# Performance work log

Hardware: AMD Instinct MI355X
Metric: run time of the kernel (lower is better)

The kernel has to match this reference:

```python
import jax, jax.numpy as jnp
import numpy as np

DIM = 1024
N_HEADS = 16
HEAD_DIM = DIM // N_HEADS
HIDDEN = 4096
EPS = 1e-12


def setup_inputs() -> dict:
    key = jax.random.key(0)
    ks = jax.random.split(key, 12)
    B, S = 2, 2048
    s = 0.02
    inp = {
        "x": jax.random.normal(ks[0], (B, S, DIM), jnp.float32),
        "attn_mask": jnp.ones((B, S), jnp.int32),
        "Wq": jax.random.normal(ks[1], (DIM, DIM), jnp.float32) * s,
        "bq": jnp.zeros((DIM,), jnp.float32),
        "Wk": jax.random.normal(ks[2], (DIM, DIM), jnp.float32) * s,
        "bk": jnp.zeros((DIM,), jnp.float32),
        "Wv": jax.random.normal(ks[3], (DIM, DIM), jnp.float32) * s,
        "bv": jnp.zeros((DIM,), jnp.float32),
        "Wo": jax.random.normal(ks[4], (DIM, DIM), jnp.float32) * s,
        "bo": jnp.zeros((DIM,), jnp.float32),
        "ln1_g": jnp.ones((DIM,), jnp.float32),
        "ln1_b": jnp.zeros((DIM,), jnp.float32),
        "W1": jax.random.normal(ks[5], (DIM, HIDDEN), jnp.float32) * s,
        "b1": jnp.zeros((HIDDEN,), jnp.float32),
        "W2": jax.random.normal(ks[6], (HIDDEN, DIM), jnp.float32) * s,
        "b2": jnp.zeros((DIM,), jnp.float32),
        "ln2_g": jnp.ones((DIM,), jnp.float32),
        "ln2_b": jnp.zeros((DIM,), jnp.float32),
    }
    return inp


def _layernorm(x, g, b):
    mu = jnp.mean(x, axis=-1, keepdims=True)
    var = jnp.mean(jnp.square(x - mu), axis=-1, keepdims=True)
    return (x - mu) * jax.lax.rsqrt(var + EPS) * g + b


def reference(x, attn_mask, Wq, bq, Wk, bk, Wv, bv, Wo, bo,
              ln1_g, ln1_b, W1, b1, W2, b2, ln2_g, ln2_b):
    B, S, D = x.shape
    def split_heads(t):  # (B,S,D) -> (B,H,S,hd)
        return t.reshape(B, S, N_HEADS, HEAD_DIM).transpose(0, 2, 1, 3)
    q = split_heads(x @ Wq + bq) * (1.0 / np.sqrt(HEAD_DIM))
    k = split_heads(x @ Wk + bk)
    v = split_heads(x @ Wv + bv)
    scores = jnp.einsum("bhqd,bhkd->bhqk", q, k)  # (B,H,S,S)
    neg = jnp.finfo(scores.dtype).min
    mask = (attn_mask == 0)[:, None, None, :]  # (B,1,1,S)
    scores = jnp.where(mask, neg, scores)
    weights = jax.nn.softmax(scores, axis=-1)
    ctx = jnp.einsum("bhqk,bhkd->bhqd", weights, v)
    ctx = ctx.transpose(0, 2, 1, 3).reshape(B, S, D)
    sa_out = ctx @ Wo + bo
    sa_out = _layernorm(sa_out + x, ln1_g, ln1_b)
    h = jax.nn.gelu(sa_out @ W1 + b1, approximate=False)
    ffn_out = h @ W2 + b2
    out = _layernorm(ffn_out + sa_out, ln2_g, ln2_b)
    return out
```

## Files before the change

### kernel.cpp

```cpp
#include <hip/hip_runtime.h>


typedef __bf16 bf16x8 __attribute__((ext_vector_type(8)));
typedef float f32x4 __attribute__((ext_vector_type(4)));

#define DIM_ 1024
#define S_LEN 2048
#define NH 16

__device__ __forceinline__ unsigned short f2bf(float f) {
  unsigned u = __float_as_uint(f);
  u = (u + 0x7FFFu + ((u >> 16) & 1u)) >> 16;
  return (unsigned short)u;
}
__device__ __forceinline__ float bf2f(unsigned short h) {
  return __uint_as_float(((unsigned)h) << 16);
}
__device__ __forceinline__ f32x4 mfma16(bf16x8 a, bf16x8 b, f32x4 c) {
  return __builtin_amdgcn_mfma_f32_16x16x32_bf16(a, b, c, 0, 0, 0);
}
__device__ __forceinline__ void gload_lds16(const void* g, void* l) {
  __builtin_amdgcn_global_load_lds(
      (const __attribute__((address_space(1))) void*)g,
      (__attribute__((address_space(3))) void*)l, 16, 0, 0);
}
__device__ __forceinline__ int swz(int row) { return ((row ^ (row >> 3)) & 7) << 3; }

__global__ __launch_bounds__(256) void trans_cvt(
    const float* __restrict__ W, unsigned short* __restrict__ Wt, int K, int N)
{
  __shared__ float tile[64][65];
  const int n0 = blockIdx.x * 64, k0 = blockIdx.y * 64;
  const int tid = threadIdx.x;
  const int tr = tid >> 4, tc = (tid & 15) << 2;
#pragma unroll
  for (int rr = 0; rr < 64; rr += 16) {
    const float4 v = *(const float4*)&W[(size_t)(k0 + tr + rr) * N + n0 + tc];
    tile[tr + rr][tc + 0] = v.x; tile[tr + rr][tc + 1] = v.y;
    tile[tr + rr][tc + 2] = v.z; tile[tr + rr][tc + 3] = v.w;
  }
  __syncthreads();
#pragma unroll
  for (int nn = 0; nn < 64; nn += 16) {
    const int n = tr + nn;
    ushort4 o;
    o.x = f2bf(tile[tc + 0][n]);
    o.y = f2bf(tile[tc + 1][n]);
    o.z = f2bf(tile[tc + 2][n]);
    o.w = f2bf(tile[tc + 3][n]);
    *(ushort4*)&Wt[(size_t)(n0 + n) * K + k0 + tc] = o;
  }
}

__global__ void cvt_bf16(const float* __restrict__ in,
                         unsigned short* __restrict__ out, int n4)
{
  const int i = blockIdx.x * blockDim.x + threadIdx.x;
  if (i >= n4) return;
  const float4 v = ((const float4*)in)[i];
  ushort4 o = { f2bf(v.x), f2bf(v.y), f2bf(v.z), f2bf(v.w) };
  ((ushort4*)out)[i] = o;
}

__global__ __launch_bounds__(256) void trans_v(
    const unsigned short* __restrict__ v, unsigned short* __restrict__ vt)
{
  __shared__ unsigned short tile[64][66];
  const int st = blockIdx.x, bh = blockIdx.y;
  const int tid = threadIdx.x;
  const int r = tid >> 3, c = (tid & 7) << 3;
  const size_t base = (size_t)bh * (S_LEN * 64);
#pragma unroll
  for (int p = 0; p < 2; ++p) {
    const int s = r + p * 32;
    const uint4 raw = *(const uint4*)(v + base + (size_t)(st * 64 + s) * 64 + c);
    const unsigned short* pr = (const unsigned short*)&raw;
#pragma unroll
    for (int j = 0; j < 8; ++j) tile[s][c + j] = pr[j];
  }
  __syncthreads();
#pragma unroll
  for (int p = 0; p < 2; ++p) {
    const int hd = r + p * 32;
    ushort4 o[2];
#pragma unroll
    for (int j = 0; j < 8; ++j) ((unsigned short*)o)[j] = tile[c + j][hd];
    *(uint4*)(vt + (size_t)bh * (64 * S_LEN) + (size_t)hd * S_LEN + st * 64 + c) =
        *(const uint4*)o;
  }
}

template <int EPI>
__global__ __launch_bounds__(256) void gemm_bt(
    const unsigned short* __restrict__ A,
    const unsigned short* __restrict__ Bt,
    const float* __restrict__ bias,
    const float* __restrict__ bias2,
    const float* __restrict__ bias3,
    int N, int K,
    unsigned short* __restrict__ bout)
{
  __shared__ __align__(16) unsigned short As[128 * 64];
  __shared__ __align__(16) unsigned short Bs[128 * 64];
  const int tn = blockIdx.x, tm = blockIdx.y;
  const int tid = threadIdx.x;
  const int wid = tid >> 6, lane = tid & 63;
  const int wm = wid >> 1, wn = wid & 1;
  const int l15 = lane & 15, lg = lane >> 4;
  const int srow = lane >> 3, sk8 = (lane & 7) << 3;

  f32x4 acc[4][4];
#pragma unroll
  for (int i = 0; i < 4; ++i)
#pragma unroll
    for (int j = 0; j < 4; ++j) acc[i][j] = (f32x4){0.f, 0.f, 0.f, 0.f};

  const size_t abase = (size_t)(tm * 128) * K;
  const size_t bbase = (size_t)(tn * 128) * K;

  for (int kk = 0; kk < K; kk += 64) {
    __syncthreads();
#pragma unroll
    for (int s = 0; s < 4; ++s) {
      const int row = wid * 32 + s * 8 + srow;
      const int sw = sk8 ^ swz(row);
      gload_lds16(A + abase + (size_t)row * K + kk + sw, &As[(wid * 32 + s * 8) * 64]);
      gload_lds16(Bt + bbase + (size_t)row * K + kk + sw, &Bs[(wid * 32 + s * 8) * 64]);
    }
    __syncthreads();
#pragma unroll
    for (int sub = 0; sub < 2; ++sub) {
      bf16x8 af[4], bfr[4];
#pragma unroll
      for (int mr = 0; mr < 4; ++mr) {
        const int row = wm * 64 + mr * 16 + l15;
        af[mr] = *(const bf16x8*)&As[row * 64 + ((sub * 32 + lg * 8) ^ swz(row))];
      }
#pragma unroll
      for (int nr = 0; nr < 4; ++nr) {
        const int row = wn * 64 + nr * 16 + l15;
        bfr[nr] = *(const bf16x8*)&Bs[row * 64 + ((sub * 32 + lg * 8) ^ swz(row))];
      }
#pragma unroll
      for (int mr = 0; mr < 4; ++mr)
#pragma unroll
        for (int nr = 0; nr < 4; ++nr)
          acc[mr][nr] = mfma16(af[mr], bfr[nr], acc[mr][nr]);
    }
  }

#pragma unroll
  for (int nr = 0; nr < 4; ++nr) {
    const int col = tn * 128 + wn * 64 + nr * 16 + l15;
    float bv;
    int which = 0, c = col;
    if (EPI == 0) {
      which = col >> 10;
      c = col & 1023;
      const float* bp = (which == 0) ? bias : (which == 1) ? bias2 : bias3;
      bv = bp[c];
    } else {
      bv = bias[col];
    }
#pragma unroll
    for (int mr = 0; mr < 4; ++mr) {
#pragma unroll
      for (int j = 0; j < 4; ++j) {
        const int row = tm * 128 + wm * 64 + mr * 16 + lg * 4 + j;
        float v = acc[mr][nr][j] + bv;
        if (EPI == 0) {
          if (which == 0) v *= 0.125f;
          const int b = row >> 11, s = row & 2047, h = c >> 6, hd = c & 63;
          bout[(size_t)which * 4194304 +
               (((size_t)(b * NH + h)) * S_LEN + s) * 64 + hd] = f2bf(v);
        } else {
          const float gl = 0.5f * v * (1.f + erff(v * 0.70710678118654752f));
          bout[(size_t)row * N + col] = f2bf(gl);
        }
      }
    }
  }
}

template <int EPI>
__global__ __launch_bounds__(256) void gemm64(
    const unsigned short* __restrict__ A,
    const unsigned short* __restrict__ Bt,
    const float* __restrict__ bias,
    int N, int K,
    float* __restrict__ fout,
    const float* __restrict__ resf,
    const unsigned short* __restrict__ resb)
{
  __shared__ __align__(16) unsigned short As[2][64 * 64];
  __shared__ __align__(16) unsigned short Bs[2][128 * 64];
  const int tn = blockIdx.x, tm = blockIdx.y;
  const int tid = threadIdx.x;
  const int wid = tid >> 6, lane = tid & 63;
  const int wm = wid >> 1, wn = wid & 1;
  const int l15 = lane & 15, lg = lane >> 4;
  const int srow = lane >> 3, sk8 = (lane & 7) << 3;

  f32x4 acc[2][4];
#pragma unroll
  for (int i = 0; i < 2; ++i)
#pragma unroll
    for (int j = 0; j < 4; ++j) acc[i][j] = (f32x4){0.f, 0.f, 0.f, 0.f};

  const size_t abase = (size_t)(tm * 64) * K;
  const size_t bbase = (size_t)(tn * 128) * K;

  auto STAGE = [&](int bufn, int kk) {
#pragma unroll
    for (int s = 0; s < 2; ++s) {
      const int row = wid * 16 + s * 8 + srow;
      gload_lds16(A + abase + (size_t)row * K + kk + (sk8 ^ swz(row)),
                  &As[bufn][(wid * 16 + s * 8) * 64]);
    }
#pragma unroll
    for (int s = 0; s < 4; ++s) {
      const int row = wid * 32 + s * 8 + srow;
      gload_lds16(Bt + bbase + (size_t)row * K + kk + (sk8 ^ swz(row)),
                  &Bs[bufn][(wid * 32 + s * 8) * 64]);
    }
  };

  STAGE(0, 0);
  __syncthreads();
  int cur = 0;
  for (int kk = 0; kk < K; kk += 64) {
    if (kk + 64 < K) STAGE(cur ^ 1, kk + 64);
#pragma unroll
    for (int sub = 0; sub < 2; ++sub) {
      bf16x8 af[2], bfr[4];
#pragma unroll
      for (int mr = 0; mr < 2; ++mr) {
        const int row = wm * 32 + mr * 16 + l15;
        af[mr] = *(const bf16x8*)&As[cur][row * 64 + ((sub * 32 + lg * 8) ^ swz(row))];
      }
#pragma unroll
      for (int nr = 0; nr < 4; ++nr) {
        const int row = wn * 64 + nr * 16 + l15;
        bfr[nr] = *(const bf16x8*)&Bs[cur][row * 64 + ((sub * 32 + lg * 8) ^ swz(row))];
      }
#pragma unroll
      for (int mr = 0; mr < 2; ++mr)
#pragma unroll
        for (int nr = 0; nr < 4; ++nr)
          acc[mr][nr] = mfma16(af[mr], bfr[nr], acc[mr][nr]);
    }
    __syncthreads();
    cur ^= 1;
  }

#pragma unroll
  for (int nr = 0; nr < 4; ++nr) {
    const int col = tn * 128 + wn * 64 + nr * 16 + l15;
    const float bv = bias[col];
#pragma unroll
    for (int mr = 0; mr < 2; ++mr) {
#pragma unroll
      for (int j = 0; j < 4; ++j) {
        const int row = tm * 64 + wm * 32 + mr * 16 + lg * 4 + j;
        const float v = acc[mr][nr][j] + bv;
        if (EPI == 1) {
          fout[(size_t)row * N + col] = v + resf[(size_t)row * N + col];
        } else {
          fout[(size_t)row * N + col] = v + bf2f(resb[(size_t)row * N + col]);
        }
      }
    }
  }
}

__global__ __launch_bounds__(512) void attn_fwd(
    const unsigned short* __restrict__ qg,
    const unsigned short* __restrict__ kg,
    const unsigned short* __restrict__ vtg,
    const int* __restrict__ amask,
    unsigned short* __restrict__ ctx)
{
  __shared__ __align__(16) unsigned short Ks[2][64 * 64];
  __shared__ __align__(16) unsigned short Vs[2][64 * 64];
  __shared__ __align__(16) unsigned short Ps[8][16 * 72];
  __shared__ int mk[2][64];

  const int bx = blockIdx.x;
  const int qt = (bx >> 3) & 15;
  const int bh = ((bx & 7) << 2) | (bx >> 7);
  const int b = bh >> 4, h = bh & 15;
  const int tid = threadIdx.x;
  const int wid = tid >> 6, lane = tid & 63;
  const int l15 = lane & 15, lg = lane >> 4;
  const int srow = lane >> 3, sk8 = (lane & 7) << 3;

  const size_t qoff =
      (((size_t)bh * S_LEN) + qt * 128 + wid * 16 + l15) * 64 + lg * 8;
  const bf16x8 aq0 = *(const bf16x8*)&qg[qoff];
  const bf16x8 aq1 = *(const bf16x8*)&qg[qoff + 32];

  f32x4 o_[4];
#pragma unroll
  for (int n = 0; n < 4; ++n) o_[n] = (f32x4){0.f, 0.f, 0.f, 0.f};
  float mj[4]  = {-3e38f, -3e38f, -3e38f, -3e38f};
  float lsj[4] = {0.f, 0.f, 0.f, 0.f};

  const size_t kbase  = (size_t)bh * (S_LEN * 64);
  const size_t vtbase = (size_t)bh * (64 * S_LEN);
  unsigned short* Pw = &Ps[wid][0];
  const int rk = wid * 8 + srow;
  const int swr = sk8 ^ swz(rk);

  auto STAGE = [&](int bufn, int t) {
    gload_lds16(kg + kbase + (size_t)(t * 64 + rk) * 64 + swr,
                &Ks[bufn][wid * 8 * 64]);
    gload_lds16(vtg + vtbase + (size_t)rk * S_LEN + t * 64 + swr,
                &Vs[bufn][wid * 8 * 64]);
    if (tid < 64) mk[bufn][tid] = amask[b * S_LEN + t * 64 + tid];
  };

  STAGE(0, 0);
  __syncthreads();
  int cur = 0;

  for (int t = 0; t < S_LEN / 64; ++t) {
    if (t + 1 < S_LEN / 64) STAGE(cur ^ 1, t + 1);

    f32x4 sf[4];
#pragma unroll
    for (int nr = 0; nr < 4; ++nr) {
      const int kvloc = nr * 16 + l15;
      const int e = swz(kvloc);
      f32x4 a = (f32x4){0.f, 0.f, 0.f, 0.f};
      const bf16x8 bk0 = *(const bf16x8*)&Ks[cur][kvloc * 64 + ((lg * 8) ^ e)];
      const bf16x8 bk1 = *(const bf16x8*)&Ks[cur][kvloc * 64 + ((32 + lg * 8) ^ e)];
      a = mfma16(aq0, bk0, a);
      a = mfma16(aq1, bk1, a);
      sf[nr] = a;
    }
#pragma unroll
    for (int nr = 0; nr < 4; ++nr)
      if (mk[cur][nr * 16 + l15] == 0)
        sf[nr] = (f32x4){-3e38f, -3e38f, -3e38f, -3e38f};

    float pv[4][4];
#pragma unroll
    for (int j = 0; j < 4; ++j) {
      float tmax = fmaxf(fmaxf(sf[0][j], sf[1][j]), fmaxf(sf[2][j], sf[3][j]));
#pragma unroll
      for (int off = 1; off < 16; off <<= 1)
        tmax = fmaxf(tmax, __shfl_xor(tmax, off));
      const float mn = fmaxf(mj[j], tmax);
      const float sc = __expf(mj[j] - mn);
      mj[j] = mn;
      lsj[j] *= sc;
      o_[0][j] *= sc; o_[1][j] *= sc; o_[2][j] *= sc; o_[3][j] *= sc;
#pragma unroll
      for (int nr = 0; nr < 4; ++nr) {
        const float p = __expf(sf[nr][j] - mn);
        pv[nr][j] = p;
        lsj[j] += p;
      }
    }

    asm volatile("s_waitcnt lgkmcnt(0)" ::: "memory");
#pragma unroll
    for (int j = 0; j < 4; ++j) {
      const int qr = lg * 4 + j;
#pragma unroll
      for (int nr = 0; nr < 4; ++nr)
        Pw[qr * 72 + nr * 16 + l15] = f2bf(pv[nr][j]);
    }
    asm volatile("s_waitcnt lgkmcnt(0)" ::: "memory");
    {
      const bf16x8 pa0 = *(const bf16x8*)&Pw[l15 * 72 + lg * 8];
      const bf16x8 pa1 = *(const bf16x8*)&Pw[l15 * 72 + 32 + lg * 8];
#pragma unroll
      for (int n = 0; n < 4; ++n) {
        const int hd = n * 16 + l15;
        const int eh = swz(hd);
        const bf16x8 bv0 = *(const bf16x8*)&Vs[cur][hd * 64 + ((lg * 8) ^ eh)];
        const bf16x8 bv1 = *(const bf16x8*)&Vs[cur][hd * 64 + ((32 + lg * 8) ^ eh)];
        o_[n] = mfma16(pa0, bv0, o_[n]);
        o_[n] = mfma16(pa1, bv1, o_[n]);
      }
    }
    __syncthreads();
    cur ^= 1;
  }

  float rinv[4];
#pragma unroll
  for (int j = 0; j < 4; ++j) {
    float s = lsj[j];
#pragma unroll
    for (int off = 1; off < 16; off <<= 1) s += __shfl_xor(s, off);
    rinv[j] = 1.f / s;
  }
#pragma unroll
  for (int n = 0; n < 4; ++n) {
#pragma unroll
    for (int j = 0; j < 4; ++j) {
      const int sr = qt * 128 + wid * 16 + lg * 4 + j;
      const size_t idx = ((size_t)b * S_LEN + sr) * DIM_ + h * 64 + n * 16 + l15;
      ctx[idx] = f2bf(o_[n][j] * rinv[j]);
    }
  }
}

template <int OUTBF>
__global__ __launch_bounds__(256) void ln_fused(
    const float* __restrict__ in, const float* __restrict__ g,
    const float* __restrict__ be,
    float* __restrict__ fout, unsigned short* __restrict__ bout)
{
  const int row = blockIdx.x, tid = threadIdx.x;
  const float4 v = ((const float4*)(in + (size_t)row * DIM_))[tid];
  float s = v.x + v.y + v.z + v.w;
  float s2 = v.x * v.x + v.y * v.y + v.z * v.z + v.w * v.w;
#pragma unroll
  for (int off = 1; off < 64; off <<= 1) {
    s += __shfl_xor(s, off);
    s2 += __shfl_xor(s2, off);
  }
  __shared__ float rs[4], rs2[4];
  if ((tid & 63) == 0) { rs[tid >> 6] = s; rs2[tid >> 6] = s2; }
  __syncthreads();
  s  = rs[0] + rs[1] + rs[2] + rs[3];
  s2 = rs2[0] + rs2[1] + rs2[2] + rs2[3];
  const float mean = s * (1.f / DIM_);
  const float var = fmaxf(s2 * (1.f / DIM_) - mean * mean, 0.f);
  const float inv = rsqrtf(var + 1e-12f);
  const float4 gv = ((const float4*)g)[tid];
  const float4 bv = ((const float4*)be)[tid];
  const float o0 = (v.x - mean) * inv * gv.x + bv.x;
  const float o1 = (v.y - mean) * inv * gv.y + bv.y;
  const float o2 = (v.z - mean) * inv * gv.z + bv.z;
  const float o3 = (v.w - mean) * inv * gv.w + bv.w;
  if (OUTBF) {
    ushort4 o = { f2bf(o0), f2bf(o1), f2bf(o2), f2bf(o3) };
    ((ushort4*)(bout + (size_t)row * DIM_))[tid] = o;
  } else {
    ((float4*)(fout + (size_t)row * DIM_))[tid] = make_float4(o0, o1, o2, o3);
  }
}

extern "C" void kernel_launch(void* const* d_in, const int* in_sizes, int n_in,
                              void* d_out, int out_size, void* d_ws, size_t ws_size,
                              hipStream_t stream)
{
  const float* x   = (const float*)d_in[0];
  const int* amask = (const int*)d_in[1];
  const float* Wq  = (const float*)d_in[2];
  const float* bq  = (const float*)d_in[3];
  const float* Wk  = (const float*)d_in[4];
  const float* bk  = (const float*)d_in[5];
  const float* Wv  = (const float*)d_in[6];
  const float* bv  = (const float*)d_in[7];
  const float* Wo  = (const float*)d_in[8];
  const float* bo  = (const float*)d_in[9];
  const float* g1  = (const float*)d_in[10];
  const float* be1 = (const float*)d_in[11];
  const float* W1  = (const float*)d_in[12];
  const float* b1  = (const float*)d_in[13];
  const float* W2  = (const float*)d_in[14];
  const float* b2  = (const float*)d_in[15];
  const float* g2  = (const float*)d_in[16];
  const float* be2 = (const float*)d_in[17];
  float* out = (float*)d_out;

  char* ws = (char*)d_ws;
  const size_t MB = (size_t)1 << 20;
  unsigned short* wqkvT = (unsigned short*)(ws + 0 * MB);
  unsigned short* wqt = wqkvT;
  unsigned short* wkt = (unsigned short*)(ws + 2 * MB);
  unsigned short* wvt = (unsigned short*)(ws + 4 * MB);
  unsigned short* wot = (unsigned short*)(ws + 6 * MB);
  unsigned short* w1t = (unsigned short*)(ws + 8 * MB);
  unsigned short* w2t = (unsigned short*)(ws + 16 * MB);
  unsigned short* qb  = (unsigned short*)(ws + 24 * MB);
  unsigned short* xb  = (unsigned short*)(ws + 48 * MB);
  unsigned short* vtb = (unsigned short*)(ws + 48 * MB);
  unsigned short* ctx = (unsigned short*)(ws + 56 * MB);
  unsigned short* sab = qb;
  unsigned short* hb  = (unsigned short*)(ws + 32 * MB);
  float* preln = out;

  trans_cvt<<<dim3(16, 16), 256, 0, stream>>>(Wq, wqt, 1024, 1024);
  trans_cvt<<<dim3(16, 16), 256, 0, stream>>>(Wk, wkt, 1024, 1024);
  trans_cvt<<<dim3(16, 16), 256, 0, stream>>>(Wv, wvt, 1024, 1024);
  trans_cvt<<<dim3(16, 16), 256, 0, stream>>>(Wo, wot, 1024, 1024);
  trans_cvt<<<dim3(64, 16), 256, 0, stream>>>(W1, w1t, 1024, 4096);
  trans_cvt<<<dim3(16, 64), 256, 0, stream>>>(W2, w2t, 4096, 1024);
  cvt_bf16<<<4096, 256, 0, stream>>>(x, xb, 4096 * 1024 / 4);

  gemm_bt<0><<<dim3(24, 32), 256, 0, stream>>>(xb, wqkvT, bq, bk, bv,
      3072, 1024, qb);

  trans_v<<<dim3(32, 32), 256, 0, stream>>>(qb + 2 * 4194304, vtb);

  attn_fwd<<<512, 512, 0, stream>>>(qb, qb + 4194304, vtb, amask, ctx);

  gemm64<1><<<dim3(8, 64), 256, 0, stream>>>(ctx, wot, bo, 1024, 1024,
      preln, x, nullptr);
  ln_fused<1><<<4096, 256, 0, stream>>>(preln, g1, be1, nullptr, sab);

  gemm_bt<2><<<dim3(32, 32), 256, 0, stream>>>(sab, w1t, b1, nullptr, nullptr,
      4096, 1024, hb);
  gemm64<3><<<dim3(8, 64), 256, 0, stream>>>(hb, w2t, b2, 1024, 4096,
      preln, nullptr, sab);
  ln_fused<0><<<4096, 256, 0, stream>>>(preln, g2, be2, out, nullptr);
}
```

Baseline: 406.4 us.

## Transpose QK^T MFMA so softmax row stats are per-lane, add lazy rescale

Swaps the operands of the QK^T MFMA so each lane holds one query row's scores. The running max and sum then need only two cross-lane shuffles instead of a 16-lane butterfly per row. The rescale of the output accumulator is skipped unless the max grows by more than a threshold. P is also stored as packed bf16x4 vectors, and s_setprio is raised around the MFMA sections. Risks are the extra shuffles needed to map per-lane scale factors back onto the O accumulator layout, and bounded precision drift from the lazy rescale threshold.

After: 395.4 us. -2.7%, faster.

```diff
diff --git a/kernel.cpp b/kernel.cpp
--- a/kernel.cpp
+++ b/kernel.cpp
@@ -2,6 +2,7 @@
 
 
 typedef __bf16 bf16x8 __attribute__((ext_vector_type(8)));
+typedef __bf16 bf16x4v __attribute__((ext_vector_type(4)));
 typedef float f32x4 __attribute__((ext_vector_type(4)));
 
 #define DIM_ 1024
@@ -283,7 +284,7 @@
   __shared__ __align__(16) unsigned short Ks[2][64 * 64];
   __shared__ __align__(16) unsigned short Vs[2][64 * 64];
   __shared__ __align__(16) unsigned short Ps[8][16 * 72];
-  __shared__ int mk[2][64];
+  __shared__ __align__(16) int mk[2][64];
 
   const int bx = blockIdx.x;
   const int qt = (bx >> 3) & 15;
@@ -302,8 +303,7 @@
   f32x4 o_[4];
 #pragma unroll
   for (int n = 0; n < 4; ++n) o_[n] = (f32x4){0.f, 0.f, 0.f, 0.f};
-  float mj[4]  = {-3e38f, -3e38f, -3e38f, -3e38f};
-  float lsj[4] = {0.f, 0.f, 0.f, 0.f};
+  float mreg = -3e38f, lsum = 0.f;
 
   const size_t kbase  = (size_t)bh * (S_LEN * 64);
   const size_t vtbase = (size_t)bh * (64 * S_LEN);
@@ -326,52 +326,69 @@
   for (int t = 0; t < S_LEN / 64; ++t) {
     if (t + 1 < S_LEN / 64) STAGE(cur ^ 1, t + 1);
 
+    __builtin_amdgcn_s_setprio(1);
     f32x4 sf[4];
 #pragma unroll
     for (int nr = 0; nr < 4; ++nr) {
       const int kvloc = nr * 16 + l15;
       const int e = swz(kvloc);
-      f32x4 a = (f32x4){0.f, 0.f, 0.f, 0.f};
       const bf16x8 bk0 = *(const bf16x8*)&Ks[cur][kvloc * 64 + ((lg * 8) ^ e)];
       const bf16x8 bk1 = *(const bf16x8*)&Ks[cur][kvloc * 64 + ((32 + lg * 8) ^ e)];
-      a = mfma16(aq0, bk0, a);
-      a = mfma16(aq1, bk1, a);
+      f32x4 a = (f32x4){0.f, 0.f, 0.f, 0.f};
+      a = mfma16(bk0, aq0, a);
+      a = mfma16(bk1, aq1, a);
       sf[nr] = a;
     }
-#pragma unroll
-    for (int nr = 0; nr < 4; ++nr)
-      if (mk[cur][nr * 16 + l15] == 0)
-        sf[nr] = (f32x4){-3e38f, -3e38f, -3e38f, -3e38f};
-
-    float pv[4][4];
-#pragma unroll
-    for (int j = 0; j < 4; ++j) {
-      float tmax = fmaxf(fmaxf(sf[0][j], sf[1][j]), fmaxf(sf[2][j], sf[3][j]));
-#pragma unroll
-      for (int off = 1; off < 16; off <<= 1)
-        tmax = fmaxf(tmax, __shfl_xor(tmax, off));
-      const float mn = fmaxf(mj[j], tmax);
-      const float sc = __expf(mj[j] - mn);
-      mj[j] = mn;
-      lsj[j] *= sc;
-      o_[0][j] *= sc; o_[1][j] *= sc; o_[2][j] *= sc; o_[3][j] *= sc;
-#pragma unroll
-      for (int nr = 0; nr < 4; ++nr) {
-        const float p = __expf(sf[nr][j] - mn);
-        pv[nr][j] = p;
-        lsj[j] += p;
+    __builtin_amdgcn_s_setprio(0);
+
+#pragma unroll
+    for (int nr = 0; nr < 4; ++nr) {
+      const int4 mki = *(const int4*)&mk[cur][nr * 16 + lg * 4];
+      if (mki.x == 0) sf[nr][0] = -3e38f;
+      if (mki.y == 0) sf[nr][1] = -3e38f;
+      if (mki.z == 0) sf[nr][2] = -3e38f;
+      if (mki.w == 0) sf[nr][3] = -3e38f;
+    }
+
+    float pmax = fmaxf(fmaxf(fmaxf(sf[0][0], sf[0][1]), fmaxf(sf[0][2], sf[0][3])),
+                       fmaxf(fmaxf(sf[1][0], sf[1][1]), fmaxf(sf[1][2], sf[1][3])));
+    pmax = fmaxf(pmax,
+           fmaxf(fmaxf(fmaxf(sf[2][0], sf[2][1]), fmaxf(sf[2][2], sf[2][3])),
+                 fmaxf(fmaxf(sf[3][0], sf[3][1]), fmaxf(sf[3][2], sf[3][3]))));
+    pmax = fmaxf(pmax, __shfl_xor(pmax, 16));
+    pmax = fmaxf(pmax, __shfl_xor(pmax, 32));
+
+    if (__any(pmax > mreg + 8.f)) {
+      const float mn = fmaxf(mreg, pmax);
+      const float sc = __expf(mreg - mn);
+      mreg = mn;
+      lsum *= sc;
+      float scr[4];
+#pragma unroll
+      for (int j = 0; j < 4; ++j) scr[j] = __shfl(sc, lg * 4 + j);
+#pragma unroll
+      for (int n = 0; n < 4; ++n) {
+        o_[n][0] *= scr[0]; o_[n][1] *= scr[1];
+        o_[n][2] *= scr[2]; o_[n][3] *= scr[3];
       }
     }
 
     asm volatile("s_waitcnt lgkmcnt(0)" ::: "memory");
 #pragma unroll
-    for (int j = 0; j < 4; ++j) {
-      const int qr = lg * 4 + j;
-#pragma unroll
-      for (int nr = 0; nr < 4; ++nr)
-        Pw[qr * 72 + nr * 16 + l15] = f2bf(pv[nr][j]);
+    for (int nr = 0; nr < 4; ++nr) {
+      const float p0 = __expf(sf[nr][0] - mreg);
+      const float p1 = __expf(sf[nr][1] - mreg);
+      const float p2 = __expf(sf[nr][2] - mreg);
+      const float p3 = __expf(sf[nr][3] - mreg);
+      lsum += (p0 + p1) + (p2 + p3);
+      bf16x4v pk;
+      pk[0] = (__bf16)p0; pk[1] = (__bf16)p1;
+      pk[2] = (__bf16)p2; pk[3] = (__bf16)p3;
+      *(bf16x4v*)&Pw[l15 * 72 + nr * 16 + lg * 4] = pk;
     }
     asm volatile("s_waitcnt lgkmcnt(0)" ::: "memory");
+
+    __builtin_amdgcn_s_setprio(1);
     {
       const bf16x8 pa0 = *(const bf16x8*)&Pw[l15 * 72 + lg * 8];
       const bf16x8 pa1 = *(const bf16x8*)&Pw[l15 * 72 + 32 + lg * 8];
@@ -385,25 +402,24 @@
         o_[n] = mfma16(pa1, bv1, o_[n]);
       }
     }
+    __builtin_amdgcn_s_setprio(0);
     __syncthreads();
     cur ^= 1;
   }
 
-  float rinv[4];
-#pragma unroll
-  for (int j = 0; j < 4; ++j) {
-    float s = lsj[j];
-#pragma unroll
-    for (int off = 1; off < 16; off <<= 1) s += __shfl_xor(s, off);
-    rinv[j] = 1.f / s;
-  }
+  lsum += __shfl_xor(lsum, 16);
+  lsum += __shfl_xor(lsum, 32);
+  const float rinv = 1.f / lsum;
+  float rj[4];
+#pragma unroll
+  for (int j = 0; j < 4; ++j) rj[j] = __shfl(rinv, lg * 4 + j);
 #pragma unroll
   for (int n = 0; n < 4; ++n) {
 #pragma unroll
     for (int j = 0; j < 4; ++j) {
       const int sr = qt * 128 + wid * 16 + lg * 4 + j;
       const size_t idx = ((size_t)b * S_LEN + sr) * DIM_ + h * 64 + n * 16 + l15;
-      ctx[idx] = f2bf(o_[n][j] * rinv[j]);
+      ctx[idx] = f2bf(o_[n][j] * rj[j]);
     }
   }
 }
```
